# Kernel tuning notes

Hardware: AMD Instinct MI355X
Metric: run time of the kernel (lower is better)

Reference implementation:

```python
import jax, jax.numpy as jnp
import numpy as np

B, C, H, W = 8, 512, 64, 64
IC = C // 2  # inter_channel


def setup_inputs() -> dict:
    key = jax.random.key(0)
    ks = jax.random.split(key, 10)
    s = 0.02
    return {
        "x": jax.random.normal(ks[0], (B, C, H, W), dtype=jnp.float32),
        "y": jax.random.normal(ks[1], (B, C, H, W), dtype=jnp.float32),
        "w_phi": jax.random.normal(ks[2], (IC, C), dtype=jnp.float32) * s,
        "b_phi": jnp.zeros((IC,), dtype=jnp.float32),
        "w_theta": jax.random.normal(ks[3], (IC, C), dtype=jnp.float32) * s,
        "b_theta": jnp.zeros((IC,), dtype=jnp.float32),
        "w_g": jax.random.normal(ks[4], (IC, C), dtype=jnp.float32) * s,
        "b_g": jnp.zeros((IC,), dtype=jnp.float32),
        "w_mask": jax.random.normal(ks[5], (C, IC), dtype=jnp.float32) * s,
        "b_mask": jnp.zeros((C,), dtype=jnp.float32),
    }


def _conv1x1(w, b, t):
    # t: [b, cin, h, w]; 1x1 conv == channel matmul
    return jnp.einsum('oc,bchw->bohw', w, t) + b[None, :, None, None]


def reference(x, y, w_phi, b_phi, w_theta, b_theta, w_g, b_g, w_mask, b_mask):
    b, c, h, w = x.shape
    ic = w_phi.shape[0]  # c // 2
    # Faithful to the torch code: conv outputs ic channels but is viewed as
    # (b, c, -1), so the sequence length is N = h*w//2 and feature dim is c.
    x_phi = _conv1x1(w_phi, b_phi, y).reshape(b, c, -1)              # [b, c, N]
    x_theta = _conv1x1(w_theta, b_theta, x).reshape(b, c, -1)
    x_theta = jnp.transpose(x_theta, (0, 2, 1))                      # [b, N, c]
    x_g = _conv1x1(w_g, b_g, x).reshape(b, c, -1)
    dict
    x_g = jnp.transpose(x_g, (0, 2, 1))                              # [b, N, c]
    scores = jnp.einsum('bnc,bcm->bnm', x_theta, x_phi)              # [b, N, N]
    attn = jax.nn.softmax(scores, axis=1)  # softmax over dim=1 (columns), as in torch
    out_nl = jnp.einsum('bnm,bmc->bnc', attn, x_g)                   # [b, N, c]
    out_nl = jnp.transpose(out_nl, (0, 2, 1)).reshape(b, ic, h, w)   # [b, ic, h, w]
    mask = _conv1x1(w_mask, b_mask, out_nl)                          # [b, c, h, w]
    return mask + x
```

## Files before the change

### kernel.cpp

```cpp
#include <hip/hip_runtime.h>
#include <hip/hip_bf16.h>


typedef __attribute__((ext_vector_type(8))) short short8;
typedef __attribute__((ext_vector_type(4))) short short4v;
typedef __attribute__((ext_vector_type(4))) float f32x4;

enum { EPI_BF16 = 0, EPI_BF16_BIAS = 1 };

__device__ __forceinline__ short f2bf(float f) {
  union { __hip_bfloat16 h; short s; } u; u.h = __float2bfloat16(f); return u.s;
}
__device__ __forceinline__ float bf2f(short s) {
  union { short s; __hip_bfloat16 h; } u; u.s = s; return __bfloat162float(u.h);
}

__device__ __forceinline__ void async_ld16(const void* g, void* l) {
  __builtin_amdgcn_global_load_lds(
      (const __attribute__((address_space(1))) unsigned int*)(unsigned long long)g,
      (__attribute__((address_space(3))) unsigned int*)(unsigned int)(unsigned long long)l,
      16, 0, 0);
}

__device__ __forceinline__ void stage_tr(const float* __restrict__ src,
                                         int kk, int px0, int s, short* Ds)
{
  const int g4 = (s >> 5) * 4;
  const int p4 = (s & 31) * 4;
  f32x4 v0 = *(const f32x4*)&src[(long)(kk + g4 + 0) * 4096 + px0 + p4];
  f32x4 v1 = *(const f32x4*)&src[(long)(kk + g4 + 1) * 4096 + px0 + p4];
  f32x4 v2 = *(const f32x4*)&src[(long)(kk + g4 + 2) * 4096 + px0 + p4];
  f32x4 v3 = *(const f32x4*)&src[(long)(kk + g4 + 3) * 4096 + px0 + p4];
  #pragma unroll
  for (int j = 0; j < 4; j++) {
    short4v w;
    w[0] = f2bf(v0[j]); w[1] = f2bf(v1[j]); w[2] = f2bf(v2[j]); w[3] = f2bf(v3[j]);
    const int px = p4 + j;
    const int u = (g4 >> 3) ^ ((px >> 2) & 3);
    *(short4v*)&Ds[px * 32 + u * 8 + (g4 & 4)] = w;
  }
}

__device__ __forceinline__ short8 frag_sw(const short* Ds, int row, int q8)
{
  return *(const short8*)&Ds[row * 32 + (((q8 >> 3) ^ ((row >> 2) & 3)) << 3)];
}

__global__ __launch_bounds__(512, 4)
void ov_k(const short* __restrict__ Eg, const short* __restrict__ Gg,
          short* __restrict__ Cg)
{
  const int L = blockIdx.x;
  const int xcd = L & 7, k = L >> 3;
  const int slab = xcd + ((k >> 2) << 3);
  const int bz = slab >> 4, by = slab & 15, bx = k & 3;

  __shared__ __align__(16) short As[128 * 32];
  __shared__ __align__(16) short Bs[128 * 32];
  const short* A = Eg + ((long)bz << 22);
  const short* B = Gg + ((long)bz << 20);
  const int m0 = by * 128;
  const int n0 = bx * 128;
  const int t = threadIdx.x;
  const int wv = t >> 6, ln = t & 63;
  const int wr = wv >> 1, wc = wv & 1;
  const int fr = ln & 15, q8 = (ln >> 4) * 8;
  const int rowA = t >> 2, kc = (t & 3) * 8;

  f32x4 acc[2][4];
  #pragma unroll
  for (int i = 0; i < 2; i++)
    #pragma unroll
    for (int j = 0; j < 4; j++)
      #pragma unroll
      for (int r = 0; r < 4; r++) acc[i][j][r] = 0.f;

  for (int kk = 0; kk < 2048; kk += 32) {
    async_ld16(A + (long)(m0 + rowA) * 2048 + kk + kc, As + wv * 512);
    async_ld16(B + (long)(n0 + rowA) * 2048 + kk + kc, Bs + wv * 512);
    __syncthreads();
    short8 af[2], bfr[4];
    #pragma unroll
    for (int mi = 0; mi < 2; mi++) af[mi] = *(const short8*)&As[(wr * 32 + mi * 16 + fr) * 32 + q8];
    #pragma unroll
    for (int ni = 0; ni < 4; ni++) bfr[ni] = *(const short8*)&Bs[(wc * 64 + ni * 16 + fr) * 32 + q8];
    #pragma unroll
    for (int mi = 0; mi < 2; mi++)
      #pragma unroll
      for (int ni = 0; ni < 4; ni++)
        acc[mi][ni] = __builtin_amdgcn_mfma_f32_16x16x32_bf16(af[mi], bfr[ni], acc[mi][ni], 0, 0, 0);
    __syncthreads();
  }

  const int colb = n0 + wc * 64 + fr;
  const int rowb = m0 + wr * 32 + (ln >> 4) * 4;
  #pragma unroll
  for (int mi = 0; mi < 2; mi++)
    #pragma unroll
    for (int r = 0; r < 4; r++) {
      const int mr = rowb + mi * 16 + r;
      #pragma unroll
      for (int ni = 0; ni < 4; ni++)
        Cg[((long)bz << 20) + (long)mr * 512 + colb + ni * 16] = f2bf(acc[mi][ni][r]);
    }
}

__global__ __launch_bounds__(256)
void conv_ptf(const float* __restrict__ x, const float* __restrict__ y,
              const short* __restrict__ wth, const short* __restrict__ wph,
              const float* __restrict__ bth, const float* __restrict__ bph,
              short* __restrict__ TPT2)
{
  __shared__ __align__(16) short As[128 * 32];
  __shared__ __align__(16) short Bs[128 * 32];
  const int m0 = blockIdx.y * 128;
  const int n0 = blockIdx.x * 128;
  const bool isphi = blockIdx.y >= 256;
  const float* src = (isphi ? y : x) + ((long)((m0 >> 12) & 7)) * (512L * 4096);
  const int px0 = m0 & 4095;
  const short* B = isphi ? wph : wth;
  const float* bias = isphi ? bph : bth;
  const int t = threadIdx.x;
  const int wv = t >> 6, ln = t & 63;
  const int wm = (wv >> 1) * 64, wn = (wv & 1) * 64;
  const int fr = ln & 15, q8 = (ln >> 4) * 8;
  const int rowA = t >> 2, kc = (t & 3) * 8;

  f32x4 acc[4][4];
  #pragma unroll
  for (int i = 0; i < 4; i++)
    #pragma unroll
    for (int j = 0; j < 4; j++)
      #pragma unroll
      for (int r = 0; r < 4; r++) acc[i][j][r] = 0.f;

  for (int kk = 0; kk < 512; kk += 32) {
    #pragma unroll
    for (int s = 0; s < 2; s++)
      async_ld16(B + (long)(n0 + s * 64 + rowA) * 512 + kk + kc, Bs + (s * 256 + wv * 64) * 8);
    stage_tr(src, kk, px0, t, As);
    __syncthreads();
    short8 af[4], bfr[4];
    #pragma unroll
    for (int mi = 0; mi < 4; mi++) af[mi] = frag_sw(As, wm + mi * 16 + fr, q8);
    #pragma unroll
    for (int ni = 0; ni < 4; ni++) bfr[ni] = *(const short8*)&Bs[(wn + ni * 16 + fr) * 32 + q8];
    #pragma unroll
    for (int mi = 0; mi < 4; mi++)
      #pragma unroll
      for (int ni = 0; ni < 4; ni++)
        acc[mi][ni] = __builtin_amdgcn_mfma_f32_16x16x32_bf16(af[mi], bfr[ni], acc[mi][ni], 0, 0, 0);
    __syncthreads();
  }

  const int colb = n0 + wn + fr;
  const int rowb = m0 + wm + (ln >> 4) * 4;
  float cb[4];
  #pragma unroll
  for (int ni = 0; ni < 4; ni++) cb[ni] = bias[colb + ni * 16];
  #pragma unroll
  for (int mi = 0; mi < 4; mi++)
    #pragma unroll
    for (int r = 0; r < 4; r++) {
      const long mr = rowb + mi * 16 + r;
      #pragma unroll
      for (int ni = 0; ni < 4; ni++)
        TPT2[mr * 256 + colb + ni * 16] = f2bf(acc[mi][ni][r] + cb[ni]);
    }
}

__global__ __launch_bounds__(512, 2)
void gemmG_f(const float* __restrict__ x, const short* __restrict__ wg,
             const float* __restrict__ bg, short* __restrict__ G)
{
  __shared__ __align__(16) short As[256 * 32];
  __shared__ __align__(16) short Bs[128 * 32];
  const int img = blockIdx.y;
  const int n0 = blockIdx.x * 128;
  const float* src = x + (long)img * 512 * 4096;
  const int t = threadIdx.x;
  const int wv = t >> 6, ln = t & 63;
  const int wr = wv >> 1, wc = wv & 1;
  const int fr = ln & 15, q8 = (ln >> 4) * 8;
  const int rowA = t >> 2, kc = (t & 3) * 8;

  f32x4 acc[4][4];
  #pragma unroll
  for (int i = 0; i < 4; i++)
    #pragma unroll
    for (int j = 0; j < 4; j++)
      #pragma unroll
      for (int r = 0; r < 4; r++) acc[i][j][r] = 0.f;

  for (int kk = 0; kk < 512; kk += 32) {
    async_ld16(wg + (long)rowA * 512 + kk + kc, As + wv * 512);
    async_ld16(wg + (long)(128 + rowA) * 512 + kk + kc, As + 4096 + wv * 512);
    if (t < 256) stage_tr(src, kk, n0, t, Bs);
    __syncthreads();
    short8 af[4], bfr[4];
    #pragma unroll
    for (int mi = 0; mi < 4; mi++) af[mi] = *(const short8*)&As[(wr * 64 + mi * 16 + fr) * 32 + q8];
    #pragma unroll
    for (int ni = 0; ni < 4; ni++) bfr[ni] = frag_sw(Bs, wc * 64 + ni * 16 + fr, q8);
    #pragma unroll
    for (int mi = 0; mi < 4; mi++)
      #pragma unroll
      for (int ni = 0; ni < 4; ni++)
        acc[mi][ni] = __builtin_amdgcn_mfma_f32_16x16x32_bf16(af[mi], bfr[ni], acc[mi][ni], 0, 0, 0);
    __syncthreads();
  }

  const int colb = n0 + wc * 64 + fr;
  const int rowb = wr * 64 + (ln >> 4) * 4;
  #pragma unroll
  for (int mi = 0; mi < 4; mi++)
    #pragma unroll
    for (int r = 0; r < 4; r++) {
      const int mr = rowb + mi * 16 + r;
      const float badd = bg[mr];
      #pragma unroll
      for (int ni = 0; ni < 4; ni++)
        G[((long)img << 20) + (long)mr * 4096 + colb + ni * 16] = f2bf(acc[mi][ni][r] + badd);
    }
}

__global__ __launch_bounds__(256)
void scores_k(const short* __restrict__ TT2, const short* __restrict__ PT2,
              short* __restrict__ ST, float* __restrict__ pstats)
{
  __shared__ __align__(16) short As[128 * 32];
  __shared__ __align__(16) short Bs[128 * 32];
  const int bz = blockIdx.z, by = blockIdx.y, bx = blockIdx.x;
  const int t = threadIdx.x;
  const int wv = t >> 6, ln = t & 63;
  const int wm = (wv >> 1) * 64, wn = (wv & 1) * 64;
  const int fr = ln & 15, q8 = (ln >> 4) * 8;
  const int rowA = t >> 2, kc = (t & 3) * 8;

  f32x4 acc[4][4];
  #pragma unroll
  for (int i = 0; i < 4; i++)
    #pragma unroll
    for (int j = 0; j < 4; j++)
      #pragma unroll
      for (int r = 0; r < 4; r++) acc[i][j][r] = 0.f;

  #pragma unroll
  for (int h = 0; h < 2; h++) {
    const short* Aseg = TT2 + ((long)(bz * 4096 + h * 2048 + by * 128)) * 256;
    const short* Bseg = PT2 + ((long)(bz * 4096 + h * 2048 + bx * 128)) * 256;
    for (int kk = 0; kk < 256; kk += 32) {
      #pragma unroll
      for (int s = 0; s < 2; s++) {
        async_ld16(Aseg + (long)(s * 64 + rowA) * 256 + kk + kc, As + (s * 256 + wv * 64) * 8);
        async_ld16(Bseg + (long)(s * 64 + rowA) * 256 + kk + kc, Bs + (s * 256 + wv * 64) * 8);
      }
      __syncthreads();
      short8 af[4], bfr[4];
      #pragma unroll
      for (int mi = 0; mi < 4; mi++) af[mi] = *(const short8*)&As[(wm + mi * 16 + fr) * 32 + q8];
      #pragma unroll
      for (int ni = 0; ni < 4; ni++) bfr[ni] = *(const short8*)&Bs[(wn + ni * 16 + fr) * 32 + q8];
      #pragma unroll
      for (int mi = 0; mi < 4; mi++)
        #pragma unroll
        for (int ni = 0; ni < 4; ni++)
          acc[mi][ni] = __builtin_amdgcn_mfma_f32_16x16x32_bf16(af[mi], bfr[ni], acc[mi][ni], 0, 0, 0);
      __syncthreads();
    }
  }

  const int colb = bx * 128 + wn + fr;
  const int rowb = by * 128 + wm + (ln >> 4) * 4;
  short* base = ST + ((long)bz << 22);
  float ps[4] = {0.f, 0.f, 0.f, 0.f};
  #pragma unroll
  for (int mi = 0; mi < 4; mi++)
    #pragma unroll
    for (int r = 0; r < 4; r++) {
      const long mr = rowb + mi * 16 + r;
      #pragma unroll
      for (int ni = 0; ni < 4; ni++) {
        float e = __expf(acc[mi][ni][r]);
        base[mr * 2048 + colb + ni * 16] = f2bf(e);
        ps[ni] += e;
      }
    }
  #pragma unroll
  for (int ni = 0; ni < 4; ni++) {
    ps[ni] += __shfl_xor(ps[ni], 16);
    ps[ni] += __shfl_xor(ps[ni], 32);
  }
  float* part = (float*)As;
  if (ln < 16) {
    #pragma unroll
    for (int ni = 0; ni < 4; ni++)
      part[(wv >> 1) * 128 + wn + ni * 16 + fr] = ps[ni];
  }
  __syncthreads();
  if (t < 128)
    pstats[((long)(bz * 16 + by)) * 2048 + bx * 128 + t] = part[t] + part[128 + t];
}

__global__ __launch_bounds__(256)
void zfinal(const float* __restrict__ pstats, float* __restrict__ invZ)
{
  const int g = blockIdx.x * 256 + threadIdx.x;
  const int b = g >> 11, col = g & 2047;
  float S = 0.f;
  #pragma unroll
  for (int rc = 0; rc < 16; rc++) S += pstats[((long)(b * 16 + rc)) * 2048 + col];
  invZ[g] = 1.f / S;
}

__global__ __launch_bounds__(256)
void g_scale(short* __restrict__ G, const float* __restrict__ invZ)
{
  const long base = ((long)blockIdx.x * 256 + threadIdx.x) * 8;
  const int bz = (int)(base >> 20);
  const int n2 = (int)(base & 4095);
  const float* z = invZ + bz * 2048 + (n2 & 2047);
  short8 v = *(short8*)&G[base];
  f32x4 z0 = *(const f32x4*)z;
  f32x4 z1 = *(const f32x4*)(z + 4);
  #pragma unroll
  for (int j = 0; j < 4; j++) { v[j] = f2bf(bf2f(v[j]) * z0[j]); v[4 + j] = f2bf(bf2f(v[4 + j]) * z1[j]); }
  *(short8*)&G[base] = v;
}

__global__ __launch_bounds__(256)
void mask_k(const short* __restrict__ Wm20, const short* __restrict__ Wm21,
            const short* __restrict__ OVT, const float* __restrict__ bmask,
            const float* __restrict__ x, float* __restrict__ out)
{
  __shared__ __align__(16) short As[128 * 32];
  __shared__ __align__(16) short Bs[128 * 32];
  const int bz = blockIdx.z;
  const int n0 = blockIdx.x * 128;
  const int m0 = blockIdx.y * 128;
  const short* A = (n0 >= 2048) ? Wm21 : Wm20;
  const short* B = OVT + ((long)bz << 20) + (long)(n0 & 2047) * 512;
  const int t = threadIdx.x;
  const int wv = t >> 6, ln = t & 63;
  const int wm = (wv >> 1) * 64, wn = (wv & 1) * 64;
  const int fr = ln & 15, q8 = (ln >> 4) * 8;
  const int rowA = t >> 2, kc = (t & 3) * 8;

  f32x4 acc[4][4];
  #pragma unroll
  for (int i = 0; i < 4; i++)
    #pragma unroll
    for (int j = 0; j < 4; j++)
      #pragma unroll
      for (int r = 0; r < 4; r++) acc[i][j][r] = 0.f;

  for (int kk = 0; kk < 512; kk += 32) {
    #pragma unroll
    for (int s = 0; s < 2; s++) {
      async_ld16(A + (long)(m0 + s * 64 + rowA) * 512 + kk + kc, As + (s * 256 + wv * 64) * 8);
      async_ld16(B + (long)(s * 64 + rowA) * 512 + kk + kc, Bs + (s * 256 + wv * 64) * 8);
    }
    __syncthreads();
    short8 af[4], bfr[4];
    #pragma unroll
    for (int mi = 0; mi < 4; mi++) af[mi] = *(const short8*)&As[(wm + mi * 16 + fr) * 32 + q8];
    #pragma unroll
    for (int ni = 0; ni < 4; ni++) bfr[ni] = *(const short8*)&Bs[(wn + ni * 16 + fr) * 32 + q8];
    #pragma unroll
    for (int mi = 0; mi < 4; mi++)
      #pragma unroll
      for (int ni = 0; ni < 4; ni++)
        acc[mi][ni] = __builtin_amdgcn_mfma_f32_16x16x32_bf16(af[mi], bfr[ni], acc[mi][ni], 0, 0, 0);
    __syncthreads();
  }

  const int colb = n0 + wn + fr;
  const int rowb = m0 + wm + (ln >> 4) * 4;
  #pragma unroll
  for (int mi = 0; mi < 4; mi++)
    #pragma unroll
    for (int r = 0; r < 4; r++) {
      const int mr = rowb + mi * 16 + r;
      const float badd = bmask[mr];
      const long rbase = ((long)bz * 512 + mr) * 4096;
      #pragma unroll
      for (int ni = 0; ni < 4; ni++) {
        const int cc = colb + ni * 16;
        out[rbase + cc] = acc[mi][ni][r] + badd + x[rbase + cc];
      }
    }
}

__global__ __launch_bounds__(256)
void wconv2(const float* w_phi, const float* w_theta, const float* w_g,
            const float* w_mask,
            short* wph, short* wth, short* wg, short* Wm20, short* Wm21)
{
  const int seg = blockIdx.x >> 6;
  const int blk = blockIdx.x & 63;
  const int i0 = blk * 2048 + threadIdx.x * 8;
  if (seg < 3) {
    const float* s = seg == 0 ? w_phi : seg == 1 ? w_theta : w_g;
    short* d = seg == 0 ? wph : seg == 1 ? wth : wg;
    f32x4 a = *(const f32x4*)&s[i0];
    f32x4 b = *(const f32x4*)&s[i0 + 4];
    short8 o;
    #pragma unroll
    for (int j = 0; j < 4; j++) { o[j] = f2bf(a[j]); o[4 + j] = f2bf(b[j]); }
    *(short8*)&d[i0] = o;
  } else {
    const int o = i0 >> 8;
    f32x4 a = *(const f32x4*)&w_mask[i0];
    f32x4 b = *(const f32x4*)&w_mask[i0 + 4];
    short v[8];
    #pragma unroll
    for (int j = 0; j < 4; j++) { v[j] = f2bf(a[j]); v[4 + j] = f2bf(b[j]); }
    short8 a0, a1, b0, b1;
    #pragma unroll
    for (int j = 0; j < 4; j++) {
      a0[2 * j] = v[j];     a0[2 * j + 1] = 0;
      a1[2 * j] = v[4 + j]; a1[2 * j + 1] = 0;
      b0[2 * j] = 0;        b0[2 * j + 1] = v[j];
      b1[2 * j] = 0;        b1[2 * j + 1] = v[4 + j];
    }
    const long base = (long)o * 512 + 2 * (i0 & 255);
    *(short8*)&Wm20[base] = a0; *(short8*)&Wm20[base + 8] = a1;
    *(short8*)&Wm21[base] = b0; *(short8*)&Wm21[base + 8] = b1;
  }
}

extern "C" void kernel_launch(void* const* d_in, const int* in_sizes, int n_in,
                              void* d_out, int out_size, void* d_ws, size_t ws_size,
                              hipStream_t stream)
{
  (void)in_sizes; (void)n_in; (void)out_size; (void)ws_size;
  const float* x       = (const float*)d_in[0];
  const float* y       = (const float*)d_in[1];
  const float* w_phi   = (const float*)d_in[2];
  const float* b_phi   = (const float*)d_in[3];
  const float* w_theta = (const float*)d_in[4];
  const float* b_theta = (const float*)d_in[5];
  const float* w_g     = (const float*)d_in[6];
  const float* b_g     = (const float*)d_in[7];
  const float* w_mask  = (const float*)d_in[8];
  const float* b_mask  = (const float*)d_in[9];
  float* out = (float*)d_out;

  char* ws = (char*)d_ws;
  const long MB = 1L << 20;
  short* wph  = (short*)(ws + 0);
  short* wth  = (short*)(ws + 256 * 1024);
  short* wg   = (short*)(ws + 512 * 1024);
  short* Wm20 = (short*)(ws + 768 * 1024);
  short* Wm21 = (short*)(ws + 1280 * 1024);
  short* TPT2 = (short*)(ws + 66 * MB);
  short* G    = (short*)(ws + 98 * MB);
  short* ST   = (short*)(ws + 2 * MB);
  float* pstats = (float*)(ws + 114 * MB);
  float* invZ   = (float*)(ws + 115 * MB);
  short* OVT  = (short*)(ws + 66 * MB);

  dim3 blk(256, 1, 1);
  dim3 blk8(512, 1, 1);

  wconv2<<<dim3(256, 1, 1), blk, 0, stream>>>(w_phi, w_theta, w_g, w_mask,
                                              wph, wth, wg, Wm20, Wm21);

  conv_ptf<<<dim3(2, 512, 1), blk, 0, stream>>>(x, y, wth, wph, b_theta, b_phi, TPT2);

  gemmG_f<<<dim3(32, 8, 1), blk8, 0, stream>>>(x, wg, b_g, G);

  scores_k<<<dim3(16, 16, 8), blk, 0, stream>>>(TPT2, TPT2 + 32768L * 256, ST, pstats);
  zfinal<<<dim3(64, 1, 1), blk, 0, stream>>>(pstats, invZ);
  g_scale<<<dim3(4096, 1, 1), blk, 0, stream>>>(G, invZ);

  ov_k<<<dim3(512, 1, 1), blk8, 0, stream>>>(ST, G, OVT);

  mask_k<<<dim3(32, 4, 8), blk, 0, stream>>>(Wm20, Wm21, OVT, b_mask, x, out);
}
```

Measured before the change: 375.5 us.

## Double-buffer and warp-specialize the conv GEMMs, widen conv_ptf tiles to all channels

Both the theta/phi conv GEMM and the G conv GEMM now use double-buffered LDS. Half the waves issue async weight loads while the other half load and transpose fp32 activations into bf16. Register loads for the next k-step are issued before the MFMAs of the current step, and one barrier per step replaces two. conv_ptf moves to 512-thread blocks that each cover all 256 output channels, so each activation slab is read once instead of twice. The cost is more LDS per block and higher register pressure under the tighter launch bounds.

```diff
diff --git a/kernel.cpp b/kernel.cpp
--- a/kernel.cpp
+++ b/kernel.cpp
@@ -5,8 +5,6 @@
 typedef __attribute__((ext_vector_type(8))) short short8;
 typedef __attribute__((ext_vector_type(4))) short short4v;
 typedef __attribute__((ext_vector_type(4))) float f32x4;
-
-enum { EPI_BF16 = 0, EPI_BF16_BIAS = 1 };
 
 __device__ __forceinline__ short f2bf(float f) {
   union { __hip_bfloat16 h; short s; } u; u.h = __float2bfloat16(f); return u.s;
@@ -20,25 +18,6 @@
       (const __attribute__((address_space(1))) unsigned int*)(unsigned long long)g,
       (__attribute__((address_space(3))) unsigned int*)(unsigned int)(unsigned long long)l,
       16, 0, 0);
-}
-
-__device__ __forceinline__ void stage_tr(const float* __restrict__ src,
-                                         int kk, int px0, int s, short* Ds)
-{
-  const int g4 = (s >> 5) * 4;
-  const int p4 = (s & 31) * 4;
-  f32x4 v0 = *(const f32x4*)&src[(long)(kk + g4 + 0) * 4096 + px0 + p4];
-  f32x4 v1 = *(const f32x4*)&src[(long)(kk + g4 + 1) * 4096 + px0 + p4];
-  f32x4 v2 = *(const f32x4*)&src[(long)(kk + g4 + 2) * 4096 + px0 + p4];
-  f32x4 v3 = *(const f32x4*)&src[(long)(kk + g4 + 3) * 4096 + px0 + p4];
-  #pragma unroll
-  for (int j = 0; j < 4; j++) {
-    short4v w;
-    w[0] = f2bf(v0[j]); w[1] = f2bf(v1[j]); w[2] = f2bf(v2[j]); w[3] = f2bf(v3[j]);
-    const int px = p4 + j;
-    const int u = (g4 >> 3) ^ ((px >> 2) & 3);
-    *(short4v*)&Ds[px * 32 + u * 8 + (g4 & 4)] = w;
-  }
 }
 
 __device__ __forceinline__ short8 frag_sw(const short* Ds, int row, int q8)
@@ -105,26 +84,28 @@
     }
 }
 
-__global__ __launch_bounds__(256)
+__global__ __launch_bounds__(512, 4)
 void conv_ptf(const float* __restrict__ x, const float* __restrict__ y,
               const short* __restrict__ wth, const short* __restrict__ wph,
               const float* __restrict__ bth, const float* __restrict__ bph,
               short* __restrict__ TPT2)
 {
-  __shared__ __align__(16) short As[128 * 32];
-  __shared__ __align__(16) short Bs[128 * 32];
-  const int m0 = blockIdx.y * 128;
-  const int n0 = blockIdx.x * 128;
-  const bool isphi = blockIdx.y >= 256;
-  const float* src = (isphi ? y : x) + ((long)((m0 >> 12) & 7)) * (512L * 4096);
-  const int px0 = m0 & 4095;
-  const short* B = isphi ? wph : wth;
+  __shared__ __align__(16) short As[2][128 * 32];
+  __shared__ __align__(16) short Bs[2][256 * 32];
+  const int slab = blockIdx.x;
+  const bool isphi = slab >= 256;
+  const int s2 = slab & 255;
+  const float* src = (isphi ? y : x) + (long)(s2 >> 5) * (512L * 4096);
+  const int px0 = (s2 & 31) * 128;
+  const long m0 = (long)slab * 128;
+  const short* W = isphi ? wph : wth;
   const float* bias = isphi ? bph : bth;
   const int t = threadIdx.x;
   const int wv = t >> 6, ln = t & 63;
-  const int wm = (wv >> 1) * 64, wn = (wv & 1) * 64;
+  const int wpx = wv >> 2, wic = wv & 3;
   const int fr = ln & 15, q8 = (ln >> 4) * 8;
-  const int rowA = t >> 2, kc = (t & 3) * 8;
+  const int g4 = (t >> 5) * 4, p4 = (t & 31) * 4;
+  const int w2 = wv - 4;
 
   f32x4 acc[4][4];
   #pragma unroll
@@ -134,47 +115,97 @@
       #pragma unroll
       for (int r = 0; r < 4; r++) acc[i][j][r] = 0.f;
 
-  for (int kk = 0; kk < 512; kk += 32) {
-    #pragma unroll
-    for (int s = 0; s < 2; s++)
-      async_ld16(B + (long)(n0 + s * 64 + rowA) * 512 + kk + kc, Bs + (s * 256 + wv * 64) * 8);
-    stage_tr(src, kk, px0, t, As);
+  if (t >= 256) {
+    #pragma unroll
+    for (int j = 0; j < 4; j++)
+      async_ld16(W + (long)(w2 * 64 + j * 16 + (ln >> 2)) * 512 + (ln & 3) * 8,
+                 &Bs[0][(w2 * 64 + j * 16) * 32]);
+  } else {
+    f32x4 r[4];
+    #pragma unroll
+    for (int i = 0; i < 4; i++)
+      r[i] = *(const f32x4*)&src[(long)(g4 + i) * 4096 + px0 + p4];
+    #pragma unroll
+    for (int j = 0; j < 4; j++) {
+      short4v w;
+      w[0] = f2bf(r[0][j]); w[1] = f2bf(r[1][j]); w[2] = f2bf(r[2][j]); w[3] = f2bf(r[3][j]);
+      const int px = p4 + j;
+      const int u = (g4 >> 3) ^ ((px >> 2) & 3);
+      *(short4v*)&As[0][px * 32 + u * 8 + (g4 & 4)] = w;
+    }
+  }
+  __syncthreads();
+
+  for (int k = 1; k < 16; k++) {
+    const int cur = (k - 1) & 1, nxt = k & 1;
+    f32x4 r[4];
+    if (t >= 256) {
+      #pragma unroll
+      for (int j = 0; j < 4; j++)
+        async_ld16(W + (long)(w2 * 64 + j * 16 + (ln >> 2)) * 512 + k * 32 + (ln & 3) * 8,
+                   &Bs[nxt][(w2 * 64 + j * 16) * 32]);
+    } else {
+      #pragma unroll
+      for (int i = 0; i < 4; i++)
+        r[i] = *(const f32x4*)&src[(long)(k * 32 + g4 + i) * 4096 + px0 + p4];
+    }
+    short8 af[4], bfv[4];
+    #pragma unroll
+    for (int mi = 0; mi < 4; mi++) af[mi] = frag_sw(&As[cur][0], wpx * 64 + mi * 16 + fr, q8);
+    #pragma unroll
+    for (int ni = 0; ni < 4; ni++) bfv[ni] = *(const short8*)&Bs[cur][(wic * 64 + ni * 16 + fr) * 32 + q8];
+    #pragma unroll
+    for (int mi = 0; mi < 4; mi++)
+      #pragma unroll
+      for (int ni = 0; ni < 4; ni++)
+        acc[mi][ni] = __builtin_amdgcn_mfma_f32_16x16x32_bf16(af[mi], bfv[ni], acc[mi][ni], 0, 0, 0);
+    if (t < 256) {
+      #pragma unroll
+      for (int j = 0; j < 4; j++) {
+        short4v w;
+        w[0] = f2bf(r[0][j]); w[1] = f2bf(r[1][j]); w[2] = f2bf(r[2][j]); w[3] = f2bf(r[3][j]);
+        const int px = p4 + j;
+        const int u = (g4 >> 3) ^ ((px >> 2) & 3);
+        *(short4v*)&As[nxt][px * 32 + u * 8 + (g4 & 4)] = w;
+      }
+    }
     __syncthreads();
-    short8 af[4], bfr[4];
-    #pragma unroll
-    for (int mi = 0; mi < 4; mi++) af[mi] = frag_sw(As, wm + mi * 16 + fr, q8);
-    #pragma unroll
-    for (int ni = 0; ni < 4; ni++) bfr[ni] = *(const short8*)&Bs[(wn + ni * 16 + fr) * 32 + q8];
+  }
+
+  {
+    short8 af[4], bfv[4];
+    #pragma unroll
+    for (int mi = 0; mi < 4; mi++) af[mi] = frag_sw(&As[1][0], wpx * 64 + mi * 16 + fr, q8);
+    #pragma unroll
+    for (int ni = 0; ni < 4; ni++) bfv[ni] = *(const short8*)&Bs[1][(wic * 64 + ni * 16 + fr) * 32 + q8];
     #pragma unroll
     for (int mi = 0; mi < 4; mi++)
       #pragma unroll
       for (int ni = 0; ni < 4; ni++)
-        acc[mi][ni] = __builtin_amdgcn_mfma_f32_16x16x32_bf16(af[mi], bfr[ni], acc[mi][ni], 0, 0, 0);
-    __syncthreads();
-  }
-
-  const int colb = n0 + wn + fr;
-  const int rowb = m0 + wm + (ln >> 4) * 4;
+        acc[mi][ni] = __builtin_amdgcn_mfma_f32_16x16x32_bf16(af[mi], bfv[ni], acc[mi][ni], 0, 0, 0);
+  }
+
+  const int colic = wic * 64 + fr;
   float cb[4];
   #pragma unroll
-  for (int ni = 0; ni < 4; ni++) cb[ni] = bias[colb + ni * 16];
+  for (int ni = 0; ni < 4; ni++) cb[ni] = bias[colic + ni * 16];
   #pragma unroll
   for (int mi = 0; mi < 4; mi++)
     #pragma unroll
     for (int r = 0; r < 4; r++) {
-      const long mr = rowb + mi * 16 + r;
-      #pragma unroll
-      for (int ni = 0; ni < 4; ni++)
-        TPT2[mr * 256 + colb + ni * 16] = f2bf(acc[mi][ni][r] + cb[ni]);
-    }
-}
-
-__global__ __launch_bounds__(512, 2)
+      const long m = m0 + wpx * 64 + mi * 16 + (ln >> 4) * 4 + r;
+      #pragma unroll
+      for (int ni = 0; ni < 4; ni++)
+        TPT2[m * 256 + colic + ni * 16] = f2bf(acc[mi][ni][r] + cb[ni]);
+    }
+}
+
+__global__ __launch_bounds__(512, 4)
 void gemmG_f(const float* __restrict__ x, const short* __restrict__ wg,
              const float* __restrict__ bg, short* __restrict__ G)
 {
-  __shared__ __align__(16) short As[256 * 32];
-  __shared__ __align__(16) short Bs[128 * 32];
+  __shared__ __align__(16) short As[2][256 * 32];
+  __shared__ __align__(16) short Bs[2][128 * 32];
   const int img = blockIdx.y;
   const int n0 = blockIdx.x * 128;
   const float* src = x + (long)img * 512 * 4096;
@@ -182,7 +213,8 @@
   const int wv = t >> 6, ln = t & 63;
   const int wr = wv >> 1, wc = wv & 1;
   const int fr = ln & 15, q8 = (ln >> 4) * 8;
-  const int rowA = t >> 2, kc = (t & 3) * 8;
+  const int g4 = (t >> 5) * 4, p4 = (t & 31) * 4;
+  const int w2 = wv - 4;
 
   f32x4 acc[4][4];
   #pragma unroll
@@ -192,22 +224,74 @@
       #pragma unroll
       for (int r = 0; r < 4; r++) acc[i][j][r] = 0.f;
 
-  for (int kk = 0; kk < 512; kk += 32) {
-    async_ld16(wg + (long)rowA * 512 + kk + kc, As + wv * 512);
-    async_ld16(wg + (long)(128 + rowA) * 512 + kk + kc, As + 4096 + wv * 512);
-    if (t < 256) stage_tr(src, kk, n0, t, Bs);
+  if (t >= 256) {
+    #pragma unroll
+    for (int j = 0; j < 4; j++)
+      async_ld16(wg + (long)(w2 * 64 + j * 16 + (ln >> 2)) * 512 + (ln & 3) * 8,
+                 &As[0][(w2 * 64 + j * 16) * 32]);
+  } else {
+    f32x4 r[4];
+    #pragma unroll
+    for (int i = 0; i < 4; i++)
+      r[i] = *(const f32x4*)&src[(long)(g4 + i) * 4096 + n0 + p4];
+    #pragma unroll
+    for (int j = 0; j < 4; j++) {
+      short4v w;
+      w[0] = f2bf(r[0][j]); w[1] = f2bf(r[1][j]); w[2] = f2bf(r[2][j]); w[3] = f2bf(r[3][j]);
+      const int px = p4 + j;
+      const int u = (g4 >> 3) ^ ((px >> 2) & 3);
+      *(short4v*)&Bs[0][px * 32 + u * 8 + (g4 & 4)] = w;
+    }
+  }
+  __syncthreads();
+
+  for (int k = 1; k < 16; k++) {
+    const int cur = (k - 1) & 1, nxt = k & 1;
+    f32x4 r[4];
+    if (t >= 256) {
+      #pragma unroll
+      for (int j = 0; j < 4; j++)
+        async_ld16(wg + (long)(w2 * 64 + j * 16 + (ln >> 2)) * 512 + k * 32 + (ln & 3) * 8,
+                   &As[nxt][(w2 * 64 + j * 16) * 32]);
+    } else {
+      #pragma unroll
+      for (int i = 0; i < 4; i++)
+        r[i] = *(const f32x4*)&src[(long)(k * 32 + g4 + i) * 4096 + n0 + p4];
+    }
+    short8 af[4], bfv[4];
+    #pragma unroll
+    for (int mi = 0; mi < 4; mi++) af[mi] = *(const short8*)&As[cur][(wr * 64 + mi * 16 + fr) * 32 + q8];
+    #pragma unroll
+    for (int ni = 0; ni < 4; ni++) bfv[ni] = frag_sw(&Bs[cur][0], wc * 64 + ni * 16 + fr, q8);
+    #pragma unroll
+    for (int mi = 0; mi < 4; mi++)
+      #pragma unroll
+      for (int ni = 0; ni < 4; ni++)
+        acc[mi][ni] = __builtin_amdgcn_mfma_f32_16x16x32_bf16(af[mi], bfv[ni], acc[mi][ni], 0, 0, 0);
+    if (t < 256) {
+      #pragma unroll
+      for (int j = 0; j < 4; j++) {
+        short4v w;
+        w[0] = f2bf(r[0][j]); w[1] = f2bf(r[1][j]); w[2] = f2bf(r[2][j]); w[3] = f2bf(r[3][j]);
+        const int px = p4 + j;
+        const int u = (g4 >> 3) ^ ((px >> 2) & 3);
+        *(short4v*)&Bs[nxt][px * 32 + u * 8 + (g4 & 4)] = w;
+      }
+    }
     __syncthreads();
-    short8 af[4], bfr[4];
-    #pragma unroll
-    for (int mi = 0; mi < 4; mi++) af[mi] = *(const short8*)&As[(wr * 64 + mi * 16 + fr) * 32 + q8];
-    #pragma unroll
-    for (int ni = 0; ni < 4; ni++) bfr[ni] = frag_sw(Bs, wc * 64 + ni * 16 + fr, q8);
+  }
+
+  {
+    short8 af[4], bfv[4];
+    #pragma unroll
+    for (int mi = 0; mi < 4; mi++) af[mi] = *(const short8*)&As[1][(wr * 64 + mi * 16 + fr) * 32 + q8];
+    #pragma unroll
+    for (int ni = 0; ni < 4; ni++) bfv[ni] = frag_sw(&Bs[1][0], wc * 64 + ni * 16 + fr, q8);
     #pragma unroll
     for (int mi = 0; mi < 4; mi++)
       #pragma unroll
       for (int ni = 0; ni < 4; ni++)
-        acc[mi][ni] = __builtin_amdgcn_mfma_f32_16x16x32_bf16(af[mi], bfr[ni], acc[mi][ni], 0, 0, 0);
-    __syncthreads();
+        acc[mi][ni] = __builtin_amdgcn_mfma_f32_16x16x32_bf16(af[mi], bfv[ni], acc[mi][ni], 0, 0, 0);
   }
 
   const int colb = n0 + wc * 64 + fr;
@@ -466,7 +550,7 @@
   wconv2<<<dim3(256, 1, 1), blk, 0, stream>>>(w_phi, w_theta, w_g, w_mask,
                                               wph, wth, wg, Wm20, Wm21);
 
-  conv_ptf<<<dim3(2, 512, 1), blk, 0, stream>>>(x, y, wth, wph, b_theta, b_phi, TPT2);
+  conv_ptf<<<dim3(512, 1, 1), blk8, 0, stream>>>(x, y, wth, wph, b_theta, b_phi, TPT2);
 
   gemmG_f<<<dim3(32, 8, 1), blk8, 0, stream>>>(x, wg, b_g, G);
 
```

Result: faster. 358.2 us (-4.6%).
